# Kernel optimization log

Measured on AMD Instinct MI355X. Metric: run time of the kernel, lower is better.

## Reference

```python
import jax, jax.numpy as jnp
import numpy as np

ALPHA = 0.5  # init alpha
B, T, D, H = 32, 1024, 512, 512


def _cell(x, h, c, wih, whh, bih, bhh):
    # PyTorch LSTM cell: gates in i, f, g, o order
    g = x @ wih.T + bih + h @ whh.T + bhh  # (B, 4H)
    i, f, gg, o = jnp.split(g, 4, axis=-1)
    c2 = jax.nn.sigmoid(f) * c + jax.nn.sigmoid(i) * jnp.tanh(gg)
    h2 = jax.nn.sigmoid(o) * jnp.tanh(c2)
    return h2, c2


def setup_inputs() -> dict:
    key = jax.random.key(0)
    ks = jax.random.split(key, 9)
    s = 1.0 / np.sqrt(H)  # torch default init scale
    u = lambda k, shp: jax.random.uniform(k, shp, jnp.float32, -s, s)
    return {
        "u_sequence": jax.random.normal(ks[0], (B, T, D), jnp.float32),
        "w_ih_f": u(ks[1], (4 * H, D)),
        "w_hh_f": u(ks[2], (4 * H, H)),
        "b_ih_f": u(ks[3], (4 * H,)),
        "b_hh_f": u(ks[4], (4 * H,)),
        "w_ih_b": u(ks[5], (4 * H, D)),
        "w_hh_b": u(ks[6], (4 * H, H)),
        "b_ih_b": u(ks[7], (4 * H,)),
        "b_hh_b": u(ks[8], (4 * H,)),
    }


def reference(u_sequence, w_ih_f, w_hh_f, b_ih_f, b_hh_f,
              w_ih_b, w_hh_b, b_ih_b, b_hh_b):
    # Per timestep the original calls the bidirectional LSTM on a length-1
    # slice: both directions reduce to a single cell step on the same input.
    # Hidden/cell state (2, B, H) is carried across timesteps.
    pf = (w_ih_f, w_hh_f, b_ih_f, b_hh_f)
    pb = (w_ih_b, w_hh_b, b_ih_b, b_hh_b)
    Bn, Tn, Dn = u_sequence.shape
    Hn = w_hh_f.shape[1]
    z = jnp.zeros((Bn, Hn), u_sequence.dtype)

    def bi_step(x, hf, cf, hb, cb):
        hf2, cf2 = _cell(x, hf, cf, *pf)
        hb2, cb2 = _cell(x, hb, cb, *pb)
        # lstm_out[:, 0, :] == concat(h_fwd, h_bwd) for seq_len == 1
        return jnp.concatenate([hf2, hb2], axis=-1), hf2, cf2, hb2, cb2

    def step(carry, u_t):  # u_t: (B, D)
        hf, cf, hb, cb = carry
        out1, hf1, cf1, hb1, cb1 = bi_step(u_t, hf, cf, hb, cb)
        x_hat = out1[:, -1:]                 # last channel scalar, (B, 1)
        x_hat_prime = u_t + x_hat            # broadcast -> (B, D)
        out2, hf2, cf2, hb2, cb2 = bi_step(x_hat_prime, hf1, cf1, hb1, cb1)
        x_hat_next = out2[:, -1:]
        out = u_t + (1.0 - ALPHA) * x_hat_prime + ALPHA * x_hat_next
        return (hf2, cf2, hb2, cb2), out

    u_tm = jnp.swapaxes(u_sequence, 0, 1)    # (T, B, D)
    _, outs = jax.lax.scan(step, (z, z, z, z), u_tm)
    return jnp.swapaxes(outs, 0, 1)          # (B, T, D)
```

## Files before the change

### kernel.cpp

```cpp
#include <hip/hip_runtime.h>
#include <cstdint>
#include <cstddef>

#define BB 32
#define TT 1024
#define DD 512
#define HH 512
#define NBLK 128

typedef __bf16 bf16x8 __attribute__((ext_vector_type(8)));
typedef float  f32x4  __attribute__((ext_vector_type(4)));
typedef unsigned long long u64;

#define HFRAG_OFF 0
#define XHAT_OFF  131072
#define IFLAG_OFF 393216
#define GCNT_OFF  394240

#define AT_LOAD(p)     __hip_atomic_load((p),      __ATOMIC_RELAXED, __HIP_MEMORY_SCOPE_AGENT)
#define AT_STORE(p, v) __hip_atomic_store((p), (v), __ATOMIC_RELAXED, __HIP_MEMORY_SCOPE_AGENT)

__device__ __forceinline__ float sigm(float x) {
    return 1.f / (1.f + __expf(-x));
}
__device__ __forceinline__ float tanh_fast(float x) {
    x = fminf(15.f, fmaxf(-15.f, x));
    float e = __expf(2.f * x);
    return (e - 1.f) / (e + 1.f);
}


__device__ __forceinline__ void arrive_flag(int* iflags, int bid) {
    __builtin_amdgcn_s_waitcnt(0);
    __syncthreads();
    if (threadIdx.x == 0) AT_STORE(&iflags[bid], 1);
}
__device__ __forceinline__ void wait_flag(const int* iflags) {
    if (threadIdx.x < 64) {
        const u64* f64 = (const u64*)iflags;
        for (;;) {
            u64 a = AT_LOAD(&f64[threadIdx.x]);
            bool ok = ((int)a >= 1) & ((int)(a >> 32) >= 1);
            if (__all(ok)) break;
            __builtin_amdgcn_s_sleep(1);
        }
    }
    __syncthreads();
}

__device__ __forceinline__ void arrive_cnt(int* gcnt, int bid) {
    __builtin_amdgcn_s_waitcnt(0);
    __syncthreads();
    if (threadIdx.x == 0)
        __hip_atomic_fetch_add(&gcnt[(bid & 7) * 16], 1,
                               __ATOMIC_RELAXED, __HIP_MEMORY_SCOPE_AGENT);
}
__device__ __forceinline__ void wait_cnt(const int* gcnt, int target) {
    if (threadIdx.x < 64) {
        const int* p = &gcnt[(threadIdx.x & 7) * 16];
        for (;;) {
            int v = AT_LOAD(p);
            if (__all(v >= target)) break;
        }
    }
    __syncthreads();
}

__global__ __launch_bounds__(256, 1) void lstm_persistent(
    const float* __restrict__ u,
    const float* __restrict__ wih_f, const float* __restrict__ whh_f,
    const float* __restrict__ bih_f, const float* __restrict__ bhh_f,
    const float* __restrict__ wih_b, const float* __restrict__ whh_b,
    const float* __restrict__ bih_b, const float* __restrict__ bhh_b,
    unsigned short* __restrict__ hfrag, float* __restrict__ xhat,
    int* __restrict__ iflags, int* __restrict__ gcnt)
{
    const int bid  = blockIdx.x;
    const int dir  = bid >> 6;
    const int kb   = bid & 63;
    const int k0   = kb << 3;
    const int tid  = threadIdx.x;
    const int wid  = tid >> 6;
    const int mi   = wid >> 1;
    const int ni   = wid & 1;
    const int lane = tid & 63;
    const int quad = lane >> 4;
    const int l16  = lane & 15;

    const float* wih = dir ? wih_b : wih_f;
    const float* whh = dir ? whh_b : whh_f;
    const float* bih = dir ? bih_b : bih_f;
    const float* bhh = dir ? bhh_b : bhh_f;

    bf16x8 wihF[16], whhF[16];
    {
        const int jg = (l16 >> 2) * HH + (k0 + 4 * mi) + (l16 & 3);
        #pragma unroll
        for (int s = 0; s < 16; ++s) {
            const float* p = wih + (size_t)jg * DD + s * 32 + quad * 8;
            const float* q = whh + (size_t)jg * HH + s * 32 + quad * 8;
            bf16x8 a, b;
            #pragma unroll
            for (int i = 0; i < 8; ++i) { a[i] = (__bf16)p[i]; b[i] = (__bf16)q[i]; }
            wihF[s] = a;
            whhF[s] = b;
        }
    }

    const int kc = k0 + 4 * mi + quad;
    const int bc = ni * 16 + l16;

    float rsv[4], biasv[4];
    {
        float rs = 0.f;
        #pragma unroll
        for (int s = 0; s < 16; ++s)
            #pragma unroll
            for (int i = 0; i < 8; ++i) rs += (float)wihF[s][i];
        rs += __shfl_xor(rs, 16);
        rs += __shfl_xor(rs, 32);
        #pragma unroll
        for (int g = 0; g < 4; ++g) {
            rsv[g]   = __shfl(rs, g * 4 + quad);
            const int j = g * HH + kc;
            biasv[g] = bih[j] + bhh[j];
        }
    }

    const int sw = kc >> 5, qw = (kc >> 3) & 3, iw = kc & 7;
    const int lanew = qw * 16 + l16;
    unsigned* hfrag32 = (unsigned*)hfrag;
    const int ws32_0 = (((((dir * 2 + 0) * 2 + ni) * 16 + sw) * 64 + lanew) * 8 + iw) >> 1;
    const int ws32_1 = ws32_0 + (2 * 16 * 64 * 8 >> 1);
    const u64* h64 = (const u64*)hfrag;
    const int rbA = ((dir * 2 + 0) * 2 + ni) * 2048 + lane * 2;
    const int rbB = ((dir * 2 + 1) * 2 + ni) * 2048 + lane * 2;

    if (!(quad & 1)) AT_STORE(&hfrag32[ws32_0], 0u);
    if (bid == 0 && tid < 8) AT_STORE(&gcnt[tid * 16], 0);

    __shared__ __align__(16) float gbuf[4][16][20];

    auto ugemm = [&](int t) -> f32x4 {
        f32x4 a0 = (f32x4){0.f, 0.f, 0.f, 0.f};
        f32x4 a1 = (f32x4){0.f, 0.f, 0.f, 0.f};
        const float* ub = u + (size_t)bc * (TT * DD) + (size_t)t * DD + quad * 8;
        #pragma unroll
        for (int s = 0; s < 16; ++s) {
            const float4* p = (const float4*)(ub + s * 32);
            float4 x0 = p[0], x1 = p[1];
            bf16x8 uf;
            uf[0] = (__bf16)x0.x; uf[1] = (__bf16)x0.y;
            uf[2] = (__bf16)x0.z; uf[3] = (__bf16)x0.w;
            uf[4] = (__bf16)x1.x; uf[5] = (__bf16)x1.y;
            uf[6] = (__bf16)x1.z; uf[7] = (__bf16)x1.w;
            if (s & 1) a1 = __builtin_amdgcn_mfma_f32_16x16x32_bf16(wihF[s], uf, a1, 0, 0, 0);
            else       a0 = __builtin_amdgcn_mfma_f32_16x16x32_bf16(wihF[s], uf, a0, 0, 0, 0);
        }
        return a0 + a1;
    };

    arrive_flag(iflags, bid);
    f32x4 gih = ugemm(0);
    wait_flag(iflags);

    float c = 0.f;
    f32x4 gnext = gih;
    int n = 1;

    for (int t = 0; t < TT; ++t) {
        #pragma unroll 1
        for (int pass = 0; pass < 2; ++pass, ++n) {
            const int bufR = (t * 2 + pass) & 1;
            float xc = 0.f;
            if (pass) xc = AT_LOAD(&xhat[t * BB + bc]);

            u64 ha[16], hb[16];
            {
                const int rb = bufR ? rbB : rbA;
                #pragma unroll
                for (int s = 0; s < 16; ++s) {
                    ha[s] = AT_LOAD(&h64[rb + s * 128]);
                    hb[s] = AT_LOAD(&h64[rb + s * 128 + 1]);
                }
            }
            f32x4 acc0 = gih;
            f32x4 acc1 = (f32x4){0.f, 0.f, 0.f, 0.f};
            #pragma unroll
            for (int s = 0; s < 16; ++s) {
                union { u64 q[2]; bf16x8 v; } cvt;
                cvt.q[0] = ha[s]; cvt.q[1] = hb[s];
                if (s & 1) acc1 = __builtin_amdgcn_mfma_f32_16x16x32_bf16(whhF[s], cvt.v, acc1, 0, 0, 0);
                else       acc0 = __builtin_amdgcn_mfma_f32_16x16x32_bf16(whhF[s], cvt.v, acc0, 0, 0, 0);
            }
            f32x4 acc = acc0 + acc1;

            float4 gw; gw.x = acc[0]; gw.y = acc[1]; gw.z = acc[2]; gw.w = acc[3];
            *(float4*)&gbuf[wid][l16][quad * 4] = gw;
            __syncthreads();
            float gI = gbuf[wid][l16][ 0 + quad] + biasv[0] + xc * rsv[0];
            float gF = gbuf[wid][l16][ 4 + quad] + biasv[1] + xc * rsv[1];
            float gG = gbuf[wid][l16][ 8 + quad] + biasv[2] + xc * rsv[2];
            float gO = gbuf[wid][l16][12 + quad] + biasv[3] + xc * rsv[3];

            float ig = sigm(gI), fg = sigm(gF), gg = tanh_fast(gG), og = sigm(gO);
            c = fg * c + ig * gg;
            float h = og * tanh_fast(c);

            float hp = __shfl_xor(h, 16);
            if (dir == 1 && kc == (HH - 1))
                AT_STORE(&xhat[pass * (TT * BB) + t * BB + bc], h);
            if (!(quad & 1)) {
                unsigned lo = (unsigned)__builtin_bit_cast(unsigned short, (__bf16)h);
                unsigned hi = (unsigned)__builtin_bit_cast(unsigned short, (__bf16)hp);
                AT_STORE(&hfrag32[bufR ? ws32_0 : ws32_1], lo | (hi << 16));
            }

            arrive_cnt(gcnt, bid);
            if (pass == 1 && t + 1 < TT)
                gnext = ugemm(t + 1);
            wait_cnt(gcnt, 16 * n);
        }
        gih = gnext;
    }
}

__global__ void epilogue(const float* __restrict__ u, const float* __restrict__ xhat,
                         float* __restrict__ out)
{
    const int i = blockIdx.x * blockDim.x + threadIdx.x;
    const float4 uv = ((const float4*)u)[i];
    const int bt = i >> 7;
    const int t = bt & (TT - 1);
    const int b = bt >> 10;
    const float s = 0.5f * (xhat[t * BB + b] + xhat[TT * BB + t * BB + b]);
    float4 o;
    o.x = 1.5f * uv.x + s;
    o.y = 1.5f * uv.y + s;
    o.z = 1.5f * uv.z + s;
    o.w = 1.5f * uv.w + s;
    ((float4*)out)[i] = o;
}

extern "C" void kernel_launch(void* const* d_in, const int* in_sizes, int n_in,
                              void* d_out, int out_size, void* d_ws, size_t ws_size,
                              hipStream_t stream) {
    const float* u     = (const float*)d_in[0];
    const float* wih_f = (const float*)d_in[1];
    const float* whh_f = (const float*)d_in[2];
    const float* bih_f = (const float*)d_in[3];
    const float* bhh_f = (const float*)d_in[4];
    const float* wih_b = (const float*)d_in[5];
    const float* whh_b = (const float*)d_in[6];
    const float* bih_b = (const float*)d_in[7];
    const float* bhh_b = (const float*)d_in[8];

    char* ws = (char*)d_ws;
    unsigned short* hfrag = (unsigned short*)(ws + HFRAG_OFF);
    float* xhat           = (float*)(ws + XHAT_OFF);
    int* iflags           = (int*)(ws + IFLAG_OFF);
    int* gcnt             = (int*)(ws + GCNT_OFF);

    lstm_persistent<<<NBLK, 256, 0, stream>>>(
        u, wih_f, whh_f, bih_f, bhh_f, wih_b, whh_b, bih_b, bhh_b,
        hfrag, xhat, iflags, gcnt);

    const int n4 = BB * TT * DD / 4;
    epilogue<<<n4 / 256, 256, 0, stream>>>(u, xhat, (float*)d_out);
}
```

Baseline: 15.50 ms.

## Split grid barrier per direction and pass xhat via flagged slot

Replaces the global atomic-counter barrier across all 128 blocks with per-block epoch flags, and each direction waits only on its own 64 blocks. The cross-direction x_hat dependency becomes a point-to-point handoff: the backward direction publishes h with a valid bit in a 64-bit slot, and consumers spin on that slot after their recurrent GEMM. This aims to cut contention on the atomics and let the two directions run decoupled. The risk is correctness if the xs slots are not cleared between launches, since stale valid bits could be read on later calls.

```diff
diff --git a/kernel.cpp b/kernel.cpp
--- a/kernel.cpp
+++ b/kernel.cpp
@@ -14,8 +14,8 @@
 
 #define HFRAG_OFF 0
 #define XHAT_OFF  131072
-#define IFLAG_OFF 393216
-#define GCNT_OFF  394240
+#define XS_OFF    393216
+#define FLAGS_OFF 655360
 
 #define AT_LOAD(p)     __hip_atomic_load((p),      __ATOMIC_RELAXED, __HIP_MEMORY_SCOPE_AGENT)
 #define AT_STORE(p, v) __hip_atomic_store((p), (v), __ATOMIC_RELAXED, __HIP_MEMORY_SCOPE_AGENT)
@@ -29,38 +29,20 @@
     return (e - 1.f) / (e + 1.f);
 }
 
-
-__device__ __forceinline__ void arrive_flag(int* iflags, int bid) {
+__device__ __forceinline__ void barrier_arrive(int* flags, int bid, int n) {
     __builtin_amdgcn_s_waitcnt(0);
     __syncthreads();
-    if (threadIdx.x == 0) AT_STORE(&iflags[bid], 1);
-}
-__device__ __forceinline__ void wait_flag(const int* iflags) {
+    if (threadIdx.x == 0) AT_STORE(&flags[bid], n);
+}
+__device__ __forceinline__ void barrier_wait(const int* flags, int dir, int n) {
     if (threadIdx.x < 64) {
-        const u64* f64 = (const u64*)iflags;
+        const u64* f64 = (const u64*)(flags + (dir << 6));
+        const int i = threadIdx.x & 31;
         for (;;) {
-            u64 a = AT_LOAD(&f64[threadIdx.x]);
-            bool ok = ((int)a >= 1) & ((int)(a >> 32) >= 1);
+            u64 a = AT_LOAD(&f64[i]);
+            bool ok = ((int)a >= n) & ((int)(a >> 32) >= n);
             if (__all(ok)) break;
             __builtin_amdgcn_s_sleep(1);
-        }
-    }
-    __syncthreads();
-}
-
-__device__ __forceinline__ void arrive_cnt(int* gcnt, int bid) {
-    __builtin_amdgcn_s_waitcnt(0);
-    __syncthreads();
-    if (threadIdx.x == 0)
-        __hip_atomic_fetch_add(&gcnt[(bid & 7) * 16], 1,
-                               __ATOMIC_RELAXED, __HIP_MEMORY_SCOPE_AGENT);
-}
-__device__ __forceinline__ void wait_cnt(const int* gcnt, int target) {
-    if (threadIdx.x < 64) {
-        const int* p = &gcnt[(threadIdx.x & 7) * 16];
-        for (;;) {
-            int v = AT_LOAD(p);
-            if (__all(v >= target)) break;
         }
     }
     __syncthreads();
@@ -73,7 +55,7 @@
     const float* __restrict__ wih_b, const float* __restrict__ whh_b,
     const float* __restrict__ bih_b, const float* __restrict__ bhh_b,
     unsigned short* __restrict__ hfrag, float* __restrict__ xhat,
-    int* __restrict__ iflags, int* __restrict__ gcnt)
+    u64* __restrict__ xs, int* __restrict__ flags)
 {
     const int bid  = blockIdx.x;
     const int dir  = bid >> 6;
@@ -137,7 +119,6 @@
     const int rbB = ((dir * 2 + 1) * 2 + ni) * 2048 + lane * 2;
 
     if (!(quad & 1)) AT_STORE(&hfrag32[ws32_0], 0u);
-    if (bid == 0 && tid < 8) AT_STORE(&gcnt[tid * 16], 0);
 
     __shared__ __align__(16) float gbuf[4][16][20];
 
@@ -160,20 +141,18 @@
         return a0 + a1;
     };
 
-    arrive_flag(iflags, bid);
+    barrier_arrive(flags, bid, 1);
     f32x4 gih = ugemm(0);
-    wait_flag(iflags);
+    barrier_wait(flags, dir, 1);
 
     float c = 0.f;
     f32x4 gnext = gih;
-    int n = 1;
+    int n = 2;
 
     for (int t = 0; t < TT; ++t) {
         #pragma unroll 1
         for (int pass = 0; pass < 2; ++pass, ++n) {
             const int bufR = (t * 2 + pass) & 1;
-            float xc = 0.f;
-            if (pass) xc = AT_LOAD(&xhat[t * BB + bc]);
 
             u64 ha[16], hb[16];
             {
@@ -195,6 +174,16 @@
             }
             f32x4 acc = acc0 + acc1;
 
+            float xc = 0.f;
+            if (pass) {
+                u64 v = AT_LOAD(&xs[t * BB + bc]);
+                while ((int)(v >> 32) < 1) {
+                    __builtin_amdgcn_s_sleep(1);
+                    v = AT_LOAD(&xs[t * BB + bc]);
+                }
+                xc = __builtin_bit_cast(float, (unsigned)v);
+            }
+
             float4 gw; gw.x = acc[0]; gw.y = acc[1]; gw.z = acc[2]; gw.w = acc[3];
             *(float4*)&gbuf[wid][l16][quad * 4] = gw;
             __syncthreads();
@@ -208,18 +197,22 @@
             float h = og * tanh_fast(c);
 
             float hp = __shfl_xor(h, 16);
-            if (dir == 1 && kc == (HH - 1))
+            if (dir == 1 && kc == (HH - 1)) {
                 AT_STORE(&xhat[pass * (TT * BB) + t * BB + bc], h);
+                if (pass == 0)
+                    AT_STORE(&xs[t * BB + bc],
+                             ((u64)1u << 32) | (u64)__builtin_bit_cast(unsigned, h));
+            }
             if (!(quad & 1)) {
                 unsigned lo = (unsigned)__builtin_bit_cast(unsigned short, (__bf16)h);
                 unsigned hi = (unsigned)__builtin_bit_cast(unsigned short, (__bf16)hp);
                 AT_STORE(&hfrag32[bufR ? ws32_0 : ws32_1], lo | (hi << 16));
             }
 
-            arrive_cnt(gcnt, bid);
+            barrier_arrive(flags, bid, n);
             if (pass == 1 && t + 1 < TT)
                 gnext = ugemm(t + 1);
-            wait_cnt(gcnt, 16 * n);
+            barrier_wait(flags, dir, n);
         }
         gih = gnext;
     }
@@ -258,12 +251,12 @@
     char* ws = (char*)d_ws;
     unsigned short* hfrag = (unsigned short*)(ws + HFRAG_OFF);
     float* xhat           = (float*)(ws + XHAT_OFF);
-    int* iflags           = (int*)(ws + IFLAG_OFF);
-    int* gcnt             = (int*)(ws + GCNT_OFF);
+    u64* xs               = (u64*)(ws + XS_OFF);
+    int* flags            = (int*)(ws + FLAGS_OFF);
 
     lstm_persistent<<<NBLK, 256, 0, stream>>>(
         u, wih_f, whh_f, bih_f, bhh_f, wih_b, whh_b, bih_b, bhh_b,
-        hfrag, xhat, iflags, gcnt);
+        hfrag, xhat, xs, flags);
 
     const int n4 = BB * TT * DD / 4;
     epilogue<<<n4 / 256, 256, 0, stream>>>(u, xhat, (float*)d_out);
```

New measurement: 15.68 ms. No clear change (+1.1%).
